# Optimization experiments

Hardware: AMD Instinct MI355X
Metric: run time of the kernel (lower is better)

The kernel has to match this reference:

```python
import jax, jax.numpy as jnp
import numpy as np

N, E = 50000, 800000
IN_DIM, HID, HEADS, OUT_DIM = 7, 64, 4, 32
EPS = 1e-5


def gat_layer(x, src, dst, W, a_s, a_d, b, heads, ch, concat):
    # x: [N, F_in]; W: [F_in, heads*ch]; a_s,a_d: [heads, ch]; b: [heads*ch] or [ch]
    n = x.shape[0]
    h = (x @ W).reshape(n, heads, ch)
    e_src = jnp.sum(h * a_s, axis=-1)  # [N, heads]
    e_dst = jnp.sum(h * a_d, axis=-1)
    e = jax.nn.leaky_relu(e_src[src] + e_dst[dst], 0.2)  # [E, heads]
    m = jax.ops.segment_max(e, dst, num_segments=n)
    ex = jnp.exp(e - m[dst])
    denom = jax.ops.segment_sum(ex, dst, num_segments=n)
    alpha = ex / (denom[dst] + 1e-16)  # [E, heads]
    msg = h[src] * alpha[:, :, None]  # [E, heads, ch]
    out = jax.ops.segment_sum(msg, dst, num_segments=n)  # [N, heads, ch]
    out = out.reshape(n, heads * ch) if concat else out.mean(axis=1)
    return out + b


def batch_norm(x, g, be):
    mu = x.mean(axis=0)
    var = x.var(axis=0)
    return (x - mu) * jax.lax.rsqrt(var + EPS) * g + be


def setup_inputs() -> dict:
    key = jax.random.key(0)
    ks = jax.random.split(key, 24)
    d = {}
    d['x'] = jax.random.normal(ks[0], (N, IN_DIM), dtype=jnp.float32)
    d['edge_index'] = jax.random.randint(ks[1], (2, E), 0, N, dtype=jnp.int32)
    d['source_node'] = 123
    s = 0.1
    HC = HEADS * HID  # 256
    d['W1'] = jax.random.normal(ks[2], (IN_DIM, HC)) * s
    d['as1'] = jax.random.normal(ks[3], (HEADS, HID)) * s
    d['ad1'] = jax.random.normal(ks[4], (HEADS, HID)) * s
    d['b1'] = jnp.zeros((HC,))
    d['g1'] = jnp.ones((HC,))
    d['be1'] = jnp.zeros((HC,))
    d['W2'] = jax.random.normal(ks[5], (HC, HC)) * s
    d['as2'] = jax.random.normal(ks[6], (HEADS, HID)) * s
    d['ad2'] = jax.random.normal(ks[7], (HEADS, HID)) * s
    d['b2'] = jnp.zeros((HC,))
    d['g2'] = jnp.ones((HC,))
    d['be2'] = jnp.zeros((HC,))
    d['W3'] = jax.random.normal(ks[8], (HC, OUT_DIM)) * s
    d['as3'] = jax.random.normal(ks[9], (1, OUT_DIM)) * s
    d['ad3'] = jax.random.normal(ks[10], (1, OUT_DIM)) * s
    d['b3'] = jnp.zeros((OUT_DIM,))
    d['Wm1'] = jax.random.normal(ks[11], (2 * OUT_DIM, 64)) * s
    d['bm1'] = jnp.zeros((64,))
    d['Wm2'] = jax.random.normal(ks[12], (64, 32)) * s
    d['bm2'] = jnp.zeros((32,))
    d['Wm3'] = jax.random.normal(ks[13], (32, 1)) * s
    d['bm3'] = jnp.zeros((1,))
    return d


def reference(x, edge_index, source_node, W1, as1, ad1, b1, g1, be1,
              W2, as2, ad2, b2, g2, be2, W3, as3, ad3, b3,
              Wm1, bm1, Wm2, bm2, Wm3, bm3):
    n = x.shape[0]
    loop = jnp.arange(n, dtype=edge_index.dtype)
    src = jnp.concatenate([edge_index[0], loop])  # PyG GATConv adds self-loops
    dst = jnp.concatenate([edge_index[1], loop])
    h = gat_layer(x, src, dst, W1, as1, ad1, b1, HEADS, HID, True)
    h = jax.nn.relu(batch_norm(h, g1, be1))
    h = gat_layer(h, src, dst, W2, as2, ad2, b2, HEADS, HID, True)
    h = jax.nn.relu(batch_norm(h, g2, be2))
    emb = gat_layer(h, src, dst, W3, as3, ad3, b3, 1, OUT_DIM, False)  # [N, 32]
    src_emb = jnp.broadcast_to(emb[source_node][None, :], (n, OUT_DIM))
    z = jnp.concatenate([src_emb, emb], axis=1)  # [N, 64]
    z = jax.nn.relu(z @ Wm1 + bm1)
    z = jax.nn.relu(z @ Wm2 + bm2)
    scores = jax.nn.sigmoid(z @ Wm3 + bm3)
    return scores.squeeze(-1)
```

## Files before the change

kernel.cpp:

```cpp
#include <hip/hip_runtime.h>
#include <hip/hip_fp16.h>
#include <math.h>

#define NN 50000
#define EE 800000
#define ETOT (EE + NN)
#define HC 256
#define HEADS 4
#define OUTD 32
#define NB1 196

typedef _Float16 f16x8 __attribute__((ext_vector_type(8)));
typedef float f32x4 __attribute__((ext_vector_type(4)));

__device__ __forceinline__ float wred_sum(float v) {
#pragma unroll
  for (int off = 32; off; off >>= 1) v += __shfl_xor(v, off);
  return v;
}
__device__ __forceinline__ float qred16(float v) {
#pragma unroll
  for (int off = 1; off < 16; off <<= 1) v += __shfl_xor(v, off);
  return v;
}
__device__ __forceinline__ float lrelu(float x) { return x >= 0.f ? x : 0.2f * x; }

__global__ void zero_i32(int* __restrict__ p, int n) {
  int i = blockIdx.x * blockDim.x + threadIdx.x;
  if (i < n) p[i] = 0;
}

__global__ void hist_k(const int* __restrict__ ei, int* __restrict__ cnt) {
  int e = blockIdx.x * blockDim.x + threadIdx.x;
  if (e >= ETOT) return;
  int d = (e < EE) ? ei[EE + e] : (e - EE);
  atomicAdd(&cnt[d], 1);
}

__global__ void scan1_k(const int* __restrict__ cnt, int* __restrict__ part,
                        int* __restrict__ bsum) {
  __shared__ int s[256];
  int t = threadIdx.x, i = blockIdx.x * 256 + t;
  int v = (i < NN) ? cnt[i] : 0;
  s[t] = v;
  __syncthreads();
#pragma unroll
  for (int off = 1; off < 256; off <<= 1) {
    int u = (t >= off) ? s[t - off] : 0;
    __syncthreads();
    s[t] += u;
    __syncthreads();
  }
  if (i < NN) part[i] = s[t] - v;
  if (t == 255) bsum[blockIdx.x] = s[255];
}

__global__ void scan2_k(const int* __restrict__ bsum, int* __restrict__ bscan) {
  __shared__ int s[256];
  int t = threadIdx.x;
  int v = (t < NB1) ? bsum[t] : 0;
  s[t] = v;
  __syncthreads();
#pragma unroll
  for (int off = 1; off < 256; off <<= 1) {
    int u = (t >= off) ? s[t - off] : 0;
    __syncthreads();
    s[t] += u;
    __syncthreads();
  }
  if (t < NB1) bscan[t] = s[t] - v;
}

__global__ void scan3_k(const int* __restrict__ part, const int* __restrict__ bscan,
                        int* __restrict__ offs, int* __restrict__ cursor) {
  int i = blockIdx.x * 256 + threadIdx.x;
  if (i < NN) {
    int v = part[i] + bscan[blockIdx.x];
    offs[i] = v;
    cursor[i] = v;
  }
  if (i == 0) offs[NN] = ETOT;
}

__global__ void scatter_k(const int* __restrict__ ei, int* __restrict__ cursor,
                          int* __restrict__ elist) {
  int e = blockIdx.x * blockDim.x + threadIdx.x;
  if (e >= ETOT) return;
  int s, d;
  if (e < EE) { s = ei[e]; d = ei[EE + e]; } else { s = d = e - EE; }
  int pos = atomicAdd(&cursor[d], 1);
  elist[pos] = s;
}

template <int NCOL>
__global__ __launch_bounds__(256) void wswz_k(const float* __restrict__ W,
                                              __half* __restrict__ Bh) {
  int idx = blockIdx.x * 256 + threadIdx.x;
  if (idx >= HC * NCOL) return;
  int k = idx / NCOL, n = idx % NCOL;
  int frag = (n >> 4) * 8 + (k >> 5);
  int lane = (n & 15) + (((k >> 3) & 3) << 4);
  int elem = k & 7;
  Bh[(frag * 64 + lane) * 8 + elem] = __float2half(W[idx]);
}

__global__ __launch_bounds__(256) void l1_h_k(
    const float* __restrict__ x, const float* __restrict__ W1,
    const float* __restrict__ asf, const float* __restrict__ adf,
    __half* __restrict__ hb, float* __restrict__ es, float* __restrict__ ed) {
  int t = threadIdx.x, w = t >> 6;
  float wc[7];
#pragma unroll
  for (int k = 0; k < 7; ++k) wc[k] = W1[k * HC + t];
  float av = asf[t], dv = adf[t];
  for (int i = blockIdx.x; i < NN; i += gridDim.x) {
    float acc = 0.f;
#pragma unroll
    for (int k = 0; k < 7; ++k) acc = fmaf(x[i * 7 + k], wc[k], acc);
    hb[(size_t)i * HC + t] = __float2half(acc);
    float a = wred_sum(acc * av);
    float d = wred_sum(acc * dv);
    if ((t & 63) == 0) { es[i * HEADS + w] = a; ed[i * HEADS + w] = d; }
  }
}

__global__ __launch_bounds__(256) void gat_agg256(
    const __half* __restrict__ hb, const float* __restrict__ es,
    const float* __restrict__ ed, const int* __restrict__ offs,
    const int* __restrict__ elist, const float* __restrict__ bias,
    __half* __restrict__ out) {
  int t = threadIdx.x, wv = t >> 6, lane = t & 63;
  int hd = lane >> 4;
  float4 bv = ((const float4*)bias)[lane];
  const float2* hb4 = (const float2*)hb;
  int i = blockIdx.x * 4 + wv;
  if (i >= NN) return;
  int base = offs[i], end = offs[i + 1];
  float edv = ed[i * HEADS + hd];
  float denom = 0.f;
  float4 acc = make_float4(0.f, 0.f, 0.f, 0.f);

#define ACC1(X_, R_)                                   \
  {                                                    \
    float2 h01_ = __half22float2(*(__half2*)&R_.x);    \
    float2 h23_ = __half22float2(*(__half2*)&R_.y);    \
    acc.x = fmaf(X_, h01_.x, acc.x);                   \
    acc.y = fmaf(X_, h01_.y, acc.y);                   \
    acc.z = fmaf(X_, h23_.x, acc.z);                   \
    acc.w = fmaf(X_, h23_.y, acc.w);                   \
  }
#define EDGE1(SRC)                                          \
  {                                                         \
    int src_ = (SRC);                                       \
    float ex_ = __expf(lrelu(es[src_ * HEADS + hd] + edv)); \
    denom += ex_;                                           \
    float2 raw_ = hb4[(size_t)src_ * 64 + lane];            \
    ACC1(ex_, raw_);                                        \
  }

  int e = base;
  int alim = (base + 3) & ~3;
  for (; e < end && e < alim; ++e) EDGE1(elist[e]);
  for (; e + 8 <= end; e += 8) {
    int4 ia = *(const int4*)&elist[e];
    int4 ib = *(const int4*)&elist[e + 4];
    float f0 = es[ia.x * HEADS + hd], f1 = es[ia.y * HEADS + hd];
    float f2 = es[ia.z * HEADS + hd], f3 = es[ia.w * HEADS + hd];
    float f4 = es[ib.x * HEADS + hd], f5 = es[ib.y * HEADS + hd];
    float f6 = es[ib.z * HEADS + hd], f7 = es[ib.w * HEADS + hd];
    float2 r0 = hb4[(size_t)ia.x * 64 + lane];
    float2 r1 = hb4[(size_t)ia.y * 64 + lane];
    float2 r2 = hb4[(size_t)ia.z * 64 + lane];
    float2 r3 = hb4[(size_t)ia.w * 64 + lane];
    float2 r4 = hb4[(size_t)ib.x * 64 + lane];
    float2 r5 = hb4[(size_t)ib.y * 64 + lane];
    float2 r6 = hb4[(size_t)ib.z * 64 + lane];
    float2 r7 = hb4[(size_t)ib.w * 64 + lane];
    float x0 = __expf(lrelu(f0 + edv)), x1 = __expf(lrelu(f1 + edv));
    float x2 = __expf(lrelu(f2 + edv)), x3 = __expf(lrelu(f3 + edv));
    float x4 = __expf(lrelu(f4 + edv)), x5 = __expf(lrelu(f5 + edv));
    float x6 = __expf(lrelu(f6 + edv)), x7 = __expf(lrelu(f7 + edv));
    denom += ((x0 + x1) + (x2 + x3)) + ((x4 + x5) + (x6 + x7));
    ACC1(x0, r0); ACC1(x1, r1); ACC1(x2, r2); ACC1(x3, r3);
    ACC1(x4, r4); ACC1(x5, r5); ACC1(x6, r6); ACC1(x7, r7);
  }
  for (; e + 4 <= end; e += 4) {
    int4 ia = *(const int4*)&elist[e];
    float f0 = es[ia.x * HEADS + hd], f1 = es[ia.y * HEADS + hd];
    float f2 = es[ia.z * HEADS + hd], f3 = es[ia.w * HEADS + hd];
    float2 r0 = hb4[(size_t)ia.x * 64 + lane];
    float2 r1 = hb4[(size_t)ia.y * 64 + lane];
    float2 r2 = hb4[(size_t)ia.z * 64 + lane];
    float2 r3 = hb4[(size_t)ia.w * 64 + lane];
    float x0 = __expf(lrelu(f0 + edv)), x1 = __expf(lrelu(f1 + edv));
    float x2 = __expf(lrelu(f2 + edv)), x3 = __expf(lrelu(f3 + edv));
    denom += (x0 + x1) + (x2 + x3);
    ACC1(x0, r0); ACC1(x1, r1); ACC1(x2, r2); ACC1(x3, r3);
  }
  for (; e < end; ++e) EDGE1(elist[e]);
#undef EDGE1
#undef ACC1

  float inv = 1.f / (denom + 1e-16f);
  __half2 o01 = __floats2half2_rn(fmaf(acc.x, inv, bv.x), fmaf(acc.y, inv, bv.y));
  __half2 o23 = __floats2half2_rn(fmaf(acc.z, inv, bv.z), fmaf(acc.w, inv, bv.w));
  uint2 pk;
  pk.x = *(unsigned int*)&o01;
  pk.y = *(unsigned int*)&o23;
  ((uint2*)(out + (size_t)i * HC))[lane] = pk;
}

__global__ __launch_bounds__(256) void bn_stats_k(const __half* __restrict__ X,
                                                  float* __restrict__ sums) {
  int t = threadIdx.x;
  int r0 = blockIdx.x * 64;
  int rend = min(r0 + 64, NN);
  float s = 0.f, q = 0.f;
  for (int r = r0; r < rend; ++r) {
    float v = __half2float(X[(size_t)r * HC + t]);
    s += v;
    q = fmaf(v, v, q);
  }
  atomicAdd(&sums[t], s);
  atomicAdd(&sums[HC + t], q);
}

__global__ void bn_final_k(const float* __restrict__ sums, const float* __restrict__ g,
                           const float* __restrict__ be, float* __restrict__ ab) {
  int t = threadIdx.x;
  float mu = sums[t] * (1.f / NN);
  float var = sums[HC + t] * (1.f / NN) - mu * mu;
  float a = g[t] * rsqrtf(var + 1e-5f);
  ab[t] = a;
  ab[HC + t] = fmaf(-mu, a, be[t]);
}

__global__ __launch_bounds__(256) void gemm_mfma_k(const __half* __restrict__ A,
                                                   const __half* __restrict__ Bh,
                                                   const float* __restrict__ ab,
                                                   const float* __restrict__ asf,
                                                   const float* __restrict__ adf,
                                                   __half* __restrict__ Ch,
                                                   float* __restrict__ es,
                                                   float* __restrict__ ed) {
  __shared__ __align__(16) __half As[128 * 40];
  __shared__ float abL[512];
  int t = threadIdx.x;
  abL[t] = ab[t];
  abL[256 + t] = ab[256 + t];
  int wv = t >> 6, lane = t & 63;
  int wm = wv >> 1, wn = wv & 1;
  int m0 = blockIdx.x * 128;
  int ntb = blockIdx.y * 8 + wn * 4;
  int srow = t >> 1;
  int skq = (t & 1) * 16;
  int grow = m0 + srow;
  const f16x8* Bf = (const f16x8*)Bh;

  f32x4 acc[4][4];
  f32x4 zf = {0.f, 0.f, 0.f, 0.f};
#pragma unroll
  for (int mt = 0; mt < 4; ++mt)
#pragma unroll
    for (int nt = 0; nt < 4; ++nt) acc[mt][nt] = zf;

  for (int ks = 0; ks < 8; ++ks) {
    int k0 = ks * 32;
    __syncthreads();
    {
      float xv[16];
      if (grow < NN) {
        const __half* ap = A + (size_t)grow * HC + k0 + skq;
        __half2 hp[8];
        *(uint4*)&hp[0] = *(const uint4*)ap;
        *(uint4*)&hp[4] = *(const uint4*)(ap + 8);
#pragma unroll
        for (int j = 0; j < 8; ++j) {
          float2 f = __half22float2(hp[j]);
          xv[2 * j] = f.x;
          xv[2 * j + 1] = f.y;
        }
      } else {
#pragma unroll
        for (int j = 0; j < 16; ++j) xv[j] = 0.f;
      }
      f16x8 v0, v1;
#pragma unroll
      for (int j = 0; j < 8; ++j) {
        float a_ = abL[k0 + skq + j], b_ = abL[256 + k0 + skq + j];
        v0[j] = (_Float16)fmaxf(fmaf(xv[j], a_, b_), 0.f);
      }
#pragma unroll
      for (int j = 0; j < 8; ++j) {
        float a_ = abL[k0 + skq + 8 + j], b_ = abL[256 + k0 + skq + 8 + j];
        v1[j] = (_Float16)fmaxf(fmaf(xv[8 + j], a_, b_), 0.f);
      }
      *(f16x8*)&As[srow * 40 + skq] = v0;
      *(f16x8*)&As[srow * 40 + skq + 8] = v1;
    }
    __syncthreads();
    f16x8 af[4], bf[4];
    int lr = wm * 64 + (lane & 15);
    int kk = (lane >> 4) * 8;
#pragma unroll
    for (int mt = 0; mt < 4; ++mt)
      af[mt] = *(const f16x8*)&As[(lr + mt * 16) * 40 + kk];
#pragma unroll
    for (int nt = 0; nt < 4; ++nt)
      bf[nt] = Bf[(size_t)((ntb + nt) * 8 + ks) * 64 + lane];
#pragma unroll
    for (int mt = 0; mt < 4; ++mt)
#pragma unroll
      for (int nt = 0; nt < 4; ++nt)
        acc[mt][nt] = __builtin_amdgcn_mfma_f32_16x16x32_f16(af[mt], bf[nt], acc[mt][nt], 0, 0, 0);
  }

  int colb = blockIdx.y * 128 + wn * 64 + (lane & 15);
#pragma unroll
  for (int mt = 0; mt < 4; ++mt) {
    int rowb = m0 + wm * 64 + mt * 16 + (lane >> 4) * 4;
#pragma unroll
    for (int nt = 0; nt < 4; ++nt) {
      int col = colb + nt * 16;
#pragma unroll
      for (int r = 0; r < 4; ++r) {
        int row = rowb + r;
        if (row < NN) Ch[(size_t)row * HC + col] = __float2half(acc[mt][nt][r]);
      }
    }
  }
  float asv[4], adv[4];
#pragma unroll
  for (int nt = 0; nt < 4; ++nt) {
    asv[nt] = asf[colb + nt * 16];
    adv[nt] = adf[colb + nt * 16];
  }
  int head = (blockIdx.y << 1) | wn;
#pragma unroll
  for (int mt = 0; mt < 4; ++mt) {
    int rowb = m0 + wm * 64 + mt * 16 + (lane >> 4) * 4;
#pragma unroll
    for (int r = 0; r < 4; ++r) {
      float pe = 0.f, pd = 0.f;
#pragma unroll
      for (int nt = 0; nt < 4; ++nt) {
        pe = fmaf(acc[mt][nt][r], asv[nt], pe);
        pd = fmaf(acc[mt][nt][r], adv[nt], pd);
      }
      pe = qred16(pe);
      pd = qred16(pd);
      int row = rowb + r;
      if ((lane & 15) == 0 && row < NN) {
        es[row * HEADS + head] = pe;
        ed[row * HEADS + head] = pd;
      }
    }
  }
}

__global__ __launch_bounds__(256) void l3_mfma_k(const __half* __restrict__ A,
                                                 const __half* __restrict__ Bh,
                                                 const float* __restrict__ ab,
                                                 const float* __restrict__ asf,
                                                 const float* __restrict__ adf,
                                                 __half* __restrict__ h3,
                                                 float* __restrict__ es3,
                                                 float* __restrict__ ed3) {
  __shared__ __align__(16) __half As[128 * 40];
  __shared__ float abL[512];
  int t = threadIdx.x;
  abL[t] = ab[t];
  abL[256 + t] = ab[256 + t];
  int wv = t >> 6, lane = t & 63;
  int m0 = blockIdx.x * 128;
  int srow = t >> 1;
  int skq = (t & 1) * 16;
  int grow = m0 + srow;
  const f16x8* Bf = (const f16x8*)Bh;

  f32x4 acc[2][2];
  f32x4 zf = {0.f, 0.f, 0.f, 0.f};
#pragma unroll
  for (int mt = 0; mt < 2; ++mt)
#pragma unroll
    for (int nt = 0; nt < 2; ++nt) acc[mt][nt] = zf;

  for (int ks = 0; ks < 8; ++ks) {
    int k0 = ks * 32;
    __syncthreads();
    {
      float xv[16];
      if (grow < NN) {
        const __half* ap = A + (size_t)grow * HC + k0 + skq;
        __half2 hp[8];
        *(uint4*)&hp[0] = *(const uint4*)ap;
        *(uint4*)&hp[4] = *(const uint4*)(ap + 8);
#pragma unroll
        for (int j = 0; j < 8; ++j) {
          float2 f = __half22float2(hp[j]);
          xv[2 * j] = f.x;
          xv[2 * j + 1] = f.y;
        }
      } else {
#pragma unroll
        for (int j = 0; j < 16; ++j) xv[j] = 0.f;
      }
      f16x8 v0, v1;
#pragma unroll
      for (int j = 0; j < 8; ++j) {
        float a_ = abL[k0 + skq + j], b_ = abL[256 + k0 + skq + j];
        v0[j] = (_Float16)fmaxf(fmaf(xv[j], a_, b_), 0.f);
      }
#pragma unroll
      for (int j = 0; j < 8; ++j) {
        float a_ = abL[k0 + skq + 8 + j], b_ = abL[256 + k0 + skq + 8 + j];
        v1[j] = (_Float16)fmaxf(fmaf(xv[8 + j], a_, b_), 0.f);
      }
      *(f16x8*)&As[srow * 40 + skq] = v0;
      *(f16x8*)&As[srow * 40 + skq + 8] = v1;
    }
    __syncthreads();
    f16x8 af[2], bf[2];
    int lr = wv * 32 + (lane & 15);
    int kk = (lane >> 4) * 8;
#pragma unroll
    for (int mt = 0; mt < 2; ++mt)
      af[mt] = *(const f16x8*)&As[(lr + mt * 16) * 40 + kk];
#pragma unroll
    for (int nt = 0; nt < 2; ++nt)
      bf[nt] = Bf[(size_t)(nt * 8 + ks) * 64 + lane];
#pragma unroll
    for (int mt = 0; mt < 2; ++mt)
#pragma unroll
      for (int nt = 0; nt < 2; ++nt)
        acc[mt][nt] = __builtin_amdgcn_mfma_f32_16x16x32_f16(af[mt], bf[nt], acc[mt][nt], 0, 0, 0);
  }

  float as3v[2], ad3v[2];
#pragma unroll
  for (int nt = 0; nt < 2; ++nt) {
    as3v[nt] = asf[nt * 16 + (lane & 15)];
    ad3v[nt] = adf[nt * 16 + (lane & 15)];
  }
#pragma unroll
  for (int mt = 0; mt < 2; ++mt) {
    int rowb = m0 + wv * 32 + mt * 16 + (lane >> 4) * 4;
#pragma unroll
    for (int r = 0; r < 4; ++r) {
      int row = rowb + r;
      float pe = 0.f, pd = 0.f;
#pragma unroll
      for (int nt = 0; nt < 2; ++nt) {
        int col = nt * 16 + (lane & 15);
        if (row < NN) h3[(size_t)row * OUTD + col] = __float2half(acc[mt][nt][r]);
        pe = fmaf(acc[mt][nt][r], as3v[nt], pe);
        pd = fmaf(acc[mt][nt][r], ad3v[nt], pd);
      }
      pe = qred16(pe);
      pd = qred16(pd);
      if ((lane & 15) == 0 && row < NN) {
        es3[row] = pe;
        ed3[row] = pd;
      }
    }
  }
}

__global__ __launch_bounds__(256) void gat_agg32(
    const __half* __restrict__ h3, const float* __restrict__ es3,
    const float* __restrict__ ed3, const int* __restrict__ offs,
    const int* __restrict__ elist, const float* __restrict__ b3,
    float* __restrict__ emb) {
  int t = threadIdx.x, wv = t >> 6, lane = t & 63;
  int eo = lane >> 5, c = lane & 31;
  float bv = b3[c];
  int i = blockIdx.x * 4 + wv;
  if (i >= NN) return;
  int base = offs[i], end = offs[i + 1];
  float edv = ed3[i];
  float denom = 0.f, acc = 0.f;
#pragma unroll 2
  for (int e = base + eo; e < end; e += 2) {
    int src = elist[e];
    float ex = __expf(lrelu(es3[src] + edv));
    denom += ex;
    acc = fmaf(ex, __half2float(h3[(size_t)src * OUTD + c]), acc);
  }
  denom += __shfl_xor(denom, 32);
  acc += __shfl_xor(acc, 32);
  if (eo == 0) emb[(size_t)i * OUTD + c] = acc / (denom + 1e-16f) + bv;
}

__global__ void c1_k(const float* __restrict__ emb, const int* __restrict__ srcn,
                     const float* __restrict__ Wm1, const float* __restrict__ bm1,
                     float* __restrict__ c1) {
  int l = threadIdx.x;
  int sn = srcn[0];
  float a = bm1[l];
  for (int k = 0; k < 32; ++k) a = fmaf(emb[(size_t)sn * OUTD + k], Wm1[k * 64 + l], a);
  c1[l] = a;
}

__global__ __launch_bounds__(256) void mlp_k(
    const float* __restrict__ emb, const float* __restrict__ c1,
    const float* __restrict__ Wm1, const float* __restrict__ Wm2,
    const float* __restrict__ bm2, const float* __restrict__ Wm3,
    const float* __restrict__ bm3, float* __restrict__ outp) {
  __shared__ float WL1s[32][64];
  __shared__ float WL2s[64][32];
  __shared__ float W3s[32];
  __shared__ float c1s[64];
  int t = threadIdx.x;
  for (int q = t; q < 2048; q += 256) WL1s[q >> 6][q & 63] = Wm1[(32 + (q >> 6)) * 64 + (q & 63)];
  for (int q = t; q < 2048; q += 256) WL2s[q >> 5][q & 31] = Wm2[q];
  if (t < 32) W3s[t] = Wm3[t];
  if (t < 64) c1s[t] = c1[t];
  __syncthreads();
  int wv = t >> 6, lane = t & 63;
  int p = lane >> 5, c = lane & 31;
  float bm2v = bm2[c];
  float bm3v = bm3[0];
  for (int node = blockIdx.x * 4 + wv; node < NN; node += gridDim.x * 4) {
    float zv = (lane < 32) ? emb[(size_t)node * OUTD + lane] : 0.f;
    float a1 = c1s[lane];
#pragma unroll
    for (int k = 0; k < 32; ++k) a1 = fmaf(__shfl(zv, k), WL1s[k][lane], a1);
    float u1 = fmaxf(a1, 0.f);
    float a2 = 0.f;
#pragma unroll
    for (int j = 0; j < 32; ++j) a2 = fmaf(__shfl(u1, p * 32 + j), WL2s[p * 32 + j][c], a2);
    a2 += __shfl_xor(a2, 32);
    float v = 0.f;
    if (lane < 32) {
      float u2 = fmaxf(a2 + bm2v, 0.f);
      v = u2 * W3s[c];
    }
    v = wred_sum(v);
    if (lane == 0) outp[node] = 1.f / (1.f + __expf(-(v + bm3v)));
  }
}

extern "C" void kernel_launch(void* const* d_in, const int* in_sizes, int n_in,
                              void* d_out, int out_size, void* d_ws, size_t ws_size,
                              hipStream_t stream) {
  const float* x   = (const float*)d_in[0];
  const int* eidx  = (const int*)d_in[1];
  const int* srcn  = (const int*)d_in[2];
  const float* W1  = (const float*)d_in[3];
  const float* as1 = (const float*)d_in[4];
  const float* ad1 = (const float*)d_in[5];
  const float* b1  = (const float*)d_in[6];
  const float* g1  = (const float*)d_in[7];
  const float* be1 = (const float*)d_in[8];
  const float* W2  = (const float*)d_in[9];
  const float* as2 = (const float*)d_in[10];
  const float* ad2 = (const float*)d_in[11];
  const float* b2  = (const float*)d_in[12];
  const float* g2  = (const float*)d_in[13];
  const float* be2 = (const float*)d_in[14];
  const float* W3  = (const float*)d_in[15];
  const float* as3 = (const float*)d_in[16];
  const float* ad3 = (const float*)d_in[17];
  const float* b3  = (const float*)d_in[18];
  const float* Wm1 = (const float*)d_in[19];
  const float* bm1 = (const float*)d_in[20];
  const float* Wm2 = (const float*)d_in[21];
  const float* bm2 = (const float*)d_in[22];
  const float* Wm3 = (const float*)d_in[23];
  const float* bm3 = (const float*)d_in[24];
  float* outp = (float*)d_out;

  char* wp = (char*)d_ws;
  auto carve = [&](size_t bytes) {
    void* p = (void*)wp;
    wp += (bytes + 255) & ~(size_t)255;
    return p;
  };
  __half* aggB  = (__half*)carve((size_t)NN * HC * 2);
  __half* hbuf  = (__half*)carve((size_t)NN * HC * 2);
  __half* h3h   = (__half*)carve((size_t)NN * OUTD * 2);
  float* emb    = (float*)carve((size_t)NN * OUTD * 4);
  float* es     = (float*)carve((size_t)NN * HEADS * 4);
  float* ed     = (float*)carve((size_t)NN * HEADS * 4);
  float* es3    = (float*)carve((size_t)NN * 4);
  float* ed3    = (float*)carve((size_t)NN * 4);
  float* bnsums = (float*)carve(2 * HC * 4);
  float* bnab   = (float*)carve(2 * HC * 4);
  float* c1     = (float*)carve(64 * 4);
  __half* Bh    = (__half*)carve((size_t)HC * HC * 2);
  __half* Bh3   = (__half*)carve((size_t)HC * OUTD * 2);
  int* offs     = (int*)carve((NN + 4) * 4);
  int* cursor   = (int*)carve(NN * 4);
  int* elist    = (int*)carve((size_t)ETOT * 4);
  int* part     = (int*)carve(NN * 4);
  int* bsum     = (int*)carve(256 * 4);
  int* bscan    = (int*)carve(256 * 4);

  const int TB = 256;
  const int gE = (ETOT + TB - 1) / TB;
  const int gN4 = (NN + 3) / 4;

  zero_i32<<<(NN + TB - 1) / TB, TB, 0, stream>>>(cursor, NN);
  hist_k<<<gE, TB, 0, stream>>>(eidx, cursor);
  scan1_k<<<NB1, TB, 0, stream>>>(cursor, part, bsum);
  scan2_k<<<1, TB, 0, stream>>>(bsum, bscan);
  scan3_k<<<NB1, TB, 0, stream>>>(part, bscan, offs, cursor);
  scatter_k<<<gE, TB, 0, stream>>>(eidx, cursor, elist);
  wswz_k<HC><<<HC * HC / TB, TB, 0, stream>>>(W2, Bh);
  wswz_k<OUTD><<<HC * OUTD / TB, TB, 0, stream>>>(W3, Bh3);

  l1_h_k<<<2048, TB, 0, stream>>>(x, W1, as1, ad1, hbuf, es, ed);
  gat_agg256<<<gN4, TB, 0, stream>>>(hbuf, es, ed, offs, elist, b1, aggB);
  zero_i32<<<2, TB, 0, stream>>>((int*)bnsums, 2 * HC);
  bn_stats_k<<<(NN + 63) / 64, TB, 0, stream>>>(aggB, bnsums);
  bn_final_k<<<1, TB, 0, stream>>>(bnsums, g1, be1, bnab);

  gemm_mfma_k<<<dim3((NN + 127) / 128, HC / 128), TB, 0, stream>>>(aggB, Bh, bnab, as2, ad2,
                                                                   hbuf, es, ed);
  gat_agg256<<<gN4, TB, 0, stream>>>(hbuf, es, ed, offs, elist, b2, aggB);
  zero_i32<<<2, TB, 0, stream>>>((int*)bnsums, 2 * HC);
  bn_stats_k<<<(NN + 63) / 64, TB, 0, stream>>>(aggB, bnsums);
  bn_final_k<<<1, TB, 0, stream>>>(bnsums, g2, be2, bnab);

  l3_mfma_k<<<(NN + 127) / 128, TB, 0, stream>>>(aggB, Bh3, bnab, as3, ad3, h3h, es3, ed3);
  gat_agg32<<<gN4, TB, 0, stream>>>(h3h, es3, ed3, offs, elist, b3, emb);

  c1_k<<<1, 64, 0, stream>>>(emb, srcn, Wm1, bm1, c1);
  mlp_k<<<512, TB, 0, stream>>>(emb, c1, Wm1, Wm2, bm2, Wm3, bm3, outp);
}
```

Before: 464.0 us.

## Fuse BN stats into aggregation, prefetch GEMM loads, rework agg32, fold c1 into MLP

```diff
diff --git a/kernel.cpp b/kernel.cpp
--- a/kernel.cpp
+++ b/kernel.cpp
@@ -128,13 +128,13 @@
     const __half* __restrict__ hb, const float* __restrict__ es,
     const float* __restrict__ ed, const int* __restrict__ offs,
     const int* __restrict__ elist, const float* __restrict__ bias,
-    __half* __restrict__ out) {
+    __half* __restrict__ out, float* __restrict__ bnsums) {
+  __shared__ float4 sA[4][64];
   int t = threadIdx.x, wv = t >> 6, lane = t & 63;
   int hd = lane >> 4;
   float4 bv = ((const float4*)bias)[lane];
   const float2* hb4 = (const float2*)hb;
   int i = blockIdx.x * 4 + wv;
-  if (i >= NN) return;
   int base = offs[i], end = offs[i + 1];
   float edv = ed[i * HEADS + hd];
   float denom = 0.f;
@@ -202,27 +202,32 @@
 #undef ACC1
 
   float inv = 1.f / (denom + 1e-16f);
-  __half2 o01 = __floats2half2_rn(fmaf(acc.x, inv, bv.x), fmaf(acc.y, inv, bv.y));
-  __half2 o23 = __floats2half2_rn(fmaf(acc.z, inv, bv.z), fmaf(acc.w, inv, bv.w));
+  float4 r;
+  r.x = fmaf(acc.x, inv, bv.x);
+  r.y = fmaf(acc.y, inv, bv.y);
+  r.z = fmaf(acc.z, inv, bv.z);
+  r.w = fmaf(acc.w, inv, bv.w);
+  __half2 o01 = __floats2half2_rn(r.x, r.y);
+  __half2 o23 = __floats2half2_rn(r.z, r.w);
   uint2 pk;
   pk.x = *(unsigned int*)&o01;
   pk.y = *(unsigned int*)&o23;
   ((uint2*)(out + (size_t)i * HC))[lane] = pk;
-}
-
-__global__ __launch_bounds__(256) void bn_stats_k(const __half* __restrict__ X,
-                                                  float* __restrict__ sums) {
-  int t = threadIdx.x;
-  int r0 = blockIdx.x * 64;
-  int rend = min(r0 + 64, NN);
-  float s = 0.f, q = 0.f;
-  for (int r = r0; r < rend; ++r) {
-    float v = __half2float(X[(size_t)r * HC + t]);
-    s += v;
-    q = fmaf(v, v, q);
-  }
-  atomicAdd(&sums[t], s);
-  atomicAdd(&sums[HC + t], q);
+
+  sA[wv][lane] = r;
+  __syncthreads();
+  {
+    int ln = t >> 2, j = t & 3;
+    const float* p0 = (const float*)&sA[0][ln];
+    const float* p1 = (const float*)&sA[1][ln];
+    const float* p2 = (const float*)&sA[2][ln];
+    const float* p3 = (const float*)&sA[3][ln];
+    float v0 = p0[j], v1 = p1[j], v2 = p2[j], v3 = p3[j];
+    float s = (v0 + v1) + (v2 + v3);
+    float q = fmaf(v0, v0, fmaf(v1, v1, fmaf(v2, v2, v3 * v3)));
+    atomicAdd(&bnsums[t], s);
+    atomicAdd(&bnsums[HC + t], q);
+  }
 }
 
 __global__ void bn_final_k(const float* __restrict__ sums, const float* __restrict__ g,
@@ -255,6 +260,8 @@
   int srow = t >> 1;
   int skq = (t & 1) * 16;
   int grow = m0 + srow;
+  bool ldok = grow < NN;
+  const __half* abase = A + (size_t)grow * HC + skq;
   const f16x8* Bf = (const f16x8*)Bh;
 
   f32x4 acc[4][4];
@@ -264,41 +271,46 @@
 #pragma unroll
     for (int nt = 0; nt < 4; ++nt) acc[mt][nt] = zf;
 
+  __half2 hp[8];
+#pragma unroll
+  for (int j = 0; j < 8; ++j) hp[j] = __half2{(__half)0.f, (__half)0.f};
+  if (ldok) {
+    *(uint4*)&hp[0] = *(const uint4*)(abase);
+    *(uint4*)&hp[4] = *(const uint4*)(abase + 8);
+  }
+
   for (int ks = 0; ks < 8; ++ks) {
     int k0 = ks * 32;
-    __syncthreads();
-    {
-      float xv[16];
-      if (grow < NN) {
-        const __half* ap = A + (size_t)grow * HC + k0 + skq;
-        __half2 hp[8];
-        *(uint4*)&hp[0] = *(const uint4*)ap;
-        *(uint4*)&hp[4] = *(const uint4*)(ap + 8);
-#pragma unroll
-        for (int j = 0; j < 8; ++j) {
-          float2 f = __half22float2(hp[j]);
-          xv[2 * j] = f.x;
-          xv[2 * j + 1] = f.y;
-        }
-      } else {
-#pragma unroll
-        for (int j = 0; j < 16; ++j) xv[j] = 0.f;
-      }
-      f16x8 v0, v1;
-#pragma unroll
-      for (int j = 0; j < 8; ++j) {
-        float a_ = abL[k0 + skq + j], b_ = abL[256 + k0 + skq + j];
-        v0[j] = (_Float16)fmaxf(fmaf(xv[j], a_, b_), 0.f);
-      }
-#pragma unroll
-      for (int j = 0; j < 8; ++j) {
-        float a_ = abL[k0 + skq + 8 + j], b_ = abL[256 + k0 + skq + 8 + j];
-        v1[j] = (_Float16)fmaxf(fmaf(xv[8 + j], a_, b_), 0.f);
-      }
-      *(f16x8*)&As[srow * 40 + skq] = v0;
-      *(f16x8*)&As[srow * 40 + skq + 8] = v1;
-    }
-    __syncthreads();
+    float xv[16];
+#pragma unroll
+    for (int j = 0; j < 8; ++j) {
+      float2 f = __half22float2(hp[j]);
+      xv[2 * j] = f.x;
+      xv[2 * j + 1] = f.y;
+    }
+    if (!ldok) {
+#pragma unroll
+      for (int j = 0; j < 16; ++j) xv[j] = 0.f;
+    }
+    f16x8 v0, v1;
+#pragma unroll
+    for (int j = 0; j < 8; ++j) {
+      float a_ = abL[k0 + skq + j], b_ = abL[256 + k0 + skq + j];
+      v0[j] = (_Float16)fmaxf(fmaf(xv[j], a_, b_), 0.f);
+    }
+#pragma unroll
+    for (int j = 0; j < 8; ++j) {
+      float a_ = abL[k0 + skq + 8 + j], b_ = abL[256 + k0 + skq + 8 + j];
+      v1[j] = (_Float16)fmaxf(fmaf(xv[8 + j], a_, b_), 0.f);
+    }
+    __syncthreads();
+    *(f16x8*)&As[srow * 40 + skq] = v0;
+    *(f16x8*)&As[srow * 40 + skq + 8] = v1;
+    __syncthreads();
+    if (ks < 7 && ldok) {
+      *(uint4*)&hp[0] = *(const uint4*)(abase + k0 + 32);
+      *(uint4*)&hp[4] = *(const uint4*)(abase + k0 + 40);
+    }
     f16x8 af[4], bf[4];
     int lr = wm * 64 + (lane & 15);
     int kk = (lane >> 4) * 8;
@@ -376,6 +388,8 @@
   int srow = t >> 1;
   int skq = (t & 1) * 16;
   int grow = m0 + srow;
+  bool ldok = grow < NN;
+  const __half* abase = A + (size_t)grow * HC + skq;
   const f16x8* Bf = (const f16x8*)Bh;
 
   f32x4 acc[2][2];
@@ -385,41 +399,46 @@
 #pragma unroll
     for (int nt = 0; nt < 2; ++nt) acc[mt][nt] = zf;
 
+  __half2 hp[8];
+#pragma unroll
+  for (int j = 0; j < 8; ++j) hp[j] = __half2{(__half)0.f, (__half)0.f};
+  if (ldok) {
+    *(uint4*)&hp[0] = *(const uint4*)(abase);
+    *(uint4*)&hp[4] = *(const uint4*)(abase + 8);
+  }
+
   for (int ks = 0; ks < 8; ++ks) {
     int k0 = ks * 32;
-    __syncthreads();
-    {
-      float xv[16];
-      if (grow < NN) {
-        const __half* ap = A + (size_t)grow * HC + k0 + skq;
-        __half2 hp[8];
-        *(uint4*)&hp[0] = *(const uint4*)ap;
-        *(uint4*)&hp[4] = *(const uint4*)(ap + 8);
-#pragma unroll
-        for (int j = 0; j < 8; ++j) {
-          float2 f = __half22float2(hp[j]);
-          xv[2 * j] = f.x;
-          xv[2 * j + 1] = f.y;
-        }
-      } else {
-#pragma unroll
-        for (int j = 0; j < 16; ++j) xv[j] = 0.f;
-      }
-      f16x8 v0, v1;
-#pragma unroll
-      for (int j = 0; j < 8; ++j) {
-        float a_ = abL[k0 + skq + j], b_ = abL[256 + k0 + skq + j];
-        v0[j] = (_Float16)fmaxf(fmaf(xv[j], a_, b_), 0.f);
-      }
-#pragma unroll
-      for (int j = 0; j < 8; ++j) {
-        float a_ = abL[k0 + skq + 8 + j], b_ = abL[256 + k0 + skq + 8 + j];
-        v1[j] = (_Float16)fmaxf(fmaf(xv[8 + j], a_, b_), 0.f);
-      }
-      *(f16x8*)&As[srow * 40 + skq] = v0;
-      *(f16x8*)&As[srow * 40 + skq + 8] = v1;
-    }
-    __syncthreads();
+    float xv[16];
+#pragma unroll
+    for (int j = 0; j < 8; ++j) {
+      float2 f = __half22float2(hp[j]);
+      xv[2 * j] = f.x;
+      xv[2 * j + 1] = f.y;
+    }
+    if (!ldok) {
+#pragma unroll
+      for (int j = 0; j < 16; ++j) xv[j] = 0.f;
+    }
+    f16x8 v0, v1;
+#pragma unroll
+    for (int j = 0; j < 8; ++j) {
+      float a_ = abL[k0 + skq + j], b_ = abL[256 + k0 + skq + j];
+      v0[j] = (_Float16)fmaxf(fmaf(xv[j], a_, b_), 0.f);
+    }
+#pragma unroll
+    for (int j = 0; j < 8; ++j) {
+      float a_ = abL[k0 + skq + 8 + j], b_ = abL[256 + k0 + skq + 8 + j];
+      v1[j] = (_Float16)fmaxf(fmaf(xv[8 + j], a_, b_), 0.f);
+    }
+    __syncthreads();
+    *(f16x8*)&As[srow * 40 + skq] = v0;
+    *(f16x8*)&As[srow * 40 + skq + 8] = v1;
+    __syncthreads();
+    if (ks < 7 && ldok) {
+      *(uint4*)&hp[0] = *(const uint4*)(abase + k0 + 32);
+      *(uint4*)&hp[4] = *(const uint4*)(abase + k0 + 40);
+    }
     f16x8 af[2], bf[2];
     int lr = wv * 32 + (lane & 15);
     int kk = (lane >> 4) * 8;
@@ -472,49 +491,76 @@
     const int* __restrict__ elist, const float* __restrict__ b3,
     float* __restrict__ emb) {
   int t = threadIdx.x, wv = t >> 6, lane = t & 63;
-  int eo = lane >> 5, c = lane & 31;
-  float bv = b3[c];
+  int g = lane >> 4, cl = lane & 15;
+  const __half2* hb2 = (const __half2*)h3;
   int i = blockIdx.x * 4 + wv;
   if (i >= NN) return;
   int base = offs[i], end = offs[i + 1];
   float edv = ed3[i];
-  float denom = 0.f, acc = 0.f;
-#pragma unroll 2
-  for (int e = base + eo; e < end; e += 2) {
-    int src = elist[e];
-    float ex = __expf(lrelu(es3[src] + edv));
-    denom += ex;
-    acc = fmaf(ex, __half2float(h3[(size_t)src * OUTD + c]), acc);
-  }
-  denom += __shfl_xor(denom, 32);
-  acc += __shfl_xor(acc, 32);
-  if (eo == 0) emb[(size_t)i * OUTD + c] = acc / (denom + 1e-16f) + bv;
-}
-
-__global__ void c1_k(const float* __restrict__ emb, const int* __restrict__ srcn,
-                     const float* __restrict__ Wm1, const float* __restrict__ bm1,
-                     float* __restrict__ c1) {
-  int l = threadIdx.x;
-  int sn = srcn[0];
-  float a = bm1[l];
-  for (int k = 0; k < 32; ++k) a = fmaf(emb[(size_t)sn * OUTD + k], Wm1[k * 64 + l], a);
-  c1[l] = a;
+  float denom = 0.f;
+  float2 acc = make_float2(0.f, 0.f);
+  int e8end = base + ((end - base) & ~7);
+  for (int e = base; e < e8end; e += 8) {
+    int e0 = e + 2 * g;
+    int s0 = elist[e0], s1 = elist[e0 + 1];
+    float f0 = es3[s0], f1 = es3[s1];
+    __half2 r0 = hb2[(size_t)s0 * 16 + cl];
+    __half2 r1 = hb2[(size_t)s1 * 16 + cl];
+    float x0 = __expf(lrelu(f0 + edv));
+    float x1 = __expf(lrelu(f1 + edv));
+    denom += x0 + x1;
+    float2 h0 = __half22float2(r0), h1 = __half22float2(r1);
+    acc.x = fmaf(x0, h0.x, fmaf(x1, h1.x, acc.x));
+    acc.y = fmaf(x0, h0.y, fmaf(x1, h1.y, acc.y));
+  }
+  for (int e = e8end + g; e < end; e += 4) {
+    int s0 = elist[e];
+    float x0 = __expf(lrelu(es3[s0] + edv));
+    __half2 r0 = hb2[(size_t)s0 * 16 + cl];
+    denom += x0;
+    float2 h0 = __half22float2(r0);
+    acc.x = fmaf(x0, h0.x, acc.x);
+    acc.y = fmaf(x0, h0.y, acc.y);
+  }
+#pragma unroll
+  for (int off = 16; off < 64; off <<= 1) {
+    denom += __shfl_xor(denom, off);
+    acc.x += __shfl_xor(acc.x, off);
+    acc.y += __shfl_xor(acc.y, off);
+  }
+  if (g == 0) {
+    float inv = 1.f / (denom + 1e-16f);
+    float2 o;
+    o.x = fmaf(acc.x, inv, b3[2 * cl]);
+    o.y = fmaf(acc.y, inv, b3[2 * cl + 1]);
+    ((float2*)(emb + (size_t)i * OUTD))[cl] = o;
+  }
 }
 
 __global__ __launch_bounds__(256) void mlp_k(
-    const float* __restrict__ emb, const float* __restrict__ c1,
-    const float* __restrict__ Wm1, const float* __restrict__ Wm2,
-    const float* __restrict__ bm2, const float* __restrict__ Wm3,
-    const float* __restrict__ bm3, float* __restrict__ outp) {
+    const float* __restrict__ emb, const int* __restrict__ srcn,
+    const float* __restrict__ Wm1, const float* __restrict__ bm1,
+    const float* __restrict__ Wm2, const float* __restrict__ bm2,
+    const float* __restrict__ Wm3, const float* __restrict__ bm3,
+    float* __restrict__ outp) {
   __shared__ float WL1s[32][64];
   __shared__ float WL2s[64][32];
   __shared__ float W3s[32];
   __shared__ float c1s[64];
+  __shared__ float zsrc[32];
   int t = threadIdx.x;
+  int sn = srcn[0];
+  if (t < 32) zsrc[t] = emb[(size_t)sn * OUTD + t];
   for (int q = t; q < 2048; q += 256) WL1s[q >> 6][q & 63] = Wm1[(32 + (q >> 6)) * 64 + (q & 63)];
   for (int q = t; q < 2048; q += 256) WL2s[q >> 5][q & 31] = Wm2[q];
   if (t < 32) W3s[t] = Wm3[t];
-  if (t < 64) c1s[t] = c1[t];
+  __syncthreads();
+  if (t < 64) {
+    float a = bm1[t];
+#pragma unroll 8
+    for (int k = 0; k < 32; ++k) a = fmaf(zsrc[k], Wm1[k * 64 + t], a);
+    c1s[t] = a;
+  }
   __syncthreads();
   int wv = t >> 6, lane = t & 63;
   int p = lane >> 5, c = lane & 31;
@@ -586,7 +632,6 @@
   float* ed3    = (float*)carve((size_t)NN * 4);
   float* bnsums = (float*)carve(2 * HC * 4);
   float* bnab   = (float*)carve(2 * HC * 4);
-  float* c1     = (float*)carve(64 * 4);
   __half* Bh    = (__half*)carve((size_t)HC * HC * 2);
   __half* Bh3   = (__half*)carve((size_t)HC * OUTD * 2);
   int* offs     = (int*)carve((NN + 4) * 4);
@@ -610,21 +655,18 @@
   wswz_k<OUTD><<<HC * OUTD / TB, TB, 0, stream>>>(W3, Bh3);
 
   l1_h_k<<<2048, TB, 0, stream>>>(x, W1, as1, ad1, hbuf, es, ed);
-  gat_agg256<<<gN4, TB, 0, stream>>>(hbuf, es, ed, offs, elist, b1, aggB);
   zero_i32<<<2, TB, 0, stream>>>((int*)bnsums, 2 * HC);
-  bn_stats_k<<<(NN + 63) / 64, TB, 0, stream>>>(aggB, bnsums);
+  gat_agg256<<<gN4, TB, 0, stream>>>(hbuf, es, ed, offs, elist, b1, aggB, bnsums);
   bn_final_k<<<1, TB, 0, stream>>>(bnsums, g1, be1, bnab);
 
   gemm_mfma_k<<<dim3((NN + 127) / 128, HC / 128), TB, 0, stream>>>(aggB, Bh, bnab, as2, ad2,
                                                                    hbuf, es, ed);
-  gat_agg256<<<gN4, TB, 0, stream>>>(hbuf, es, ed, offs, elist, b2, aggB);
   zero_i32<<<2, TB, 0, stream>>>((int*)bnsums, 2 * HC);
-  bn_stats_k<<<(NN + 63) / 64, TB, 0, stream>>>(aggB, bnsums);
+  gat_agg256<<<gN4, TB, 0, stream>>>(hbuf, es, ed, offs, elist, b2, aggB, bnsums);
   bn_final_k<<<1, TB, 0, stream>>>(bnsums, g2, be2, bnab);
 
   l3_mfma_k<<<(NN + 127) / 128, TB, 0, stream>>>(aggB, Bh3, bnab, as3, ad3, h3h, es3, ed3);
   gat_agg32<<<gN4, TB, 0, stream>>>(h3h, es3, ed3, offs, elist, b3, emb);
 
-  c1_k<<<1, 64, 0, stream>>>(emb, srcn, Wm1, bm1, c1);
-  mlp_k<<<512, TB, 0, stream>>>(emb, c1, Wm1, Wm2, bm2, Wm3, bm3, outp);
-}
+  mlp_k<<<512, TB, 0, stream>>>(emb, srcn, Wm1, bm1, Wm2, bm2, Wm3, bm3, outp);
+}
```

Measured after the change: 883.4 us. 90.4% more time.
